# Kernel optimization log

Measured on AMD Instinct MI355X. Metric: run time of the kernel, lower is better.

The kernel has to match this reference:

```python
import jax, jax.numpy as jnp
import numpy as np

B, D, K, P = 512, 2048, 128, 5

def setup_inputs() -> dict:
    key = jax.random.key(0)
    k1, k2 = jax.random.split(key)
    x = jax.random.normal(k1, (B, D), dtype=jnp.float32)
    theta = 0.05 * jax.random.normal(k2, (D, K, P), dtype=jnp.float32)
    log_weight_scale = jnp.zeros((K, P), dtype=jnp.float32)
    bias = -jnp.ones((K,), dtype=jnp.float32)  # layer inits bias to -1
    return {"x": x, "theta": theta, "log_weight_scale": log_weight_scale, "bias": bias}

def reference(x, theta, log_weight_scale, bias):
    b = x.shape[0]
    # weight-normalized kernel: [D, K, P]
    norm = jnp.sqrt(jnp.sum(theta * theta, axis=0))            # [K, P]
    kernel = theta * (jnp.exp(log_weight_scale) / norm)[None]  # [D, K, P]
    actv = jnp.einsum('bd,dkp->bkp', x, kernel)                # [B, K, P]
    # pairwise L1 over P: [B, K, B]
    diff = jnp.abs(actv[:, :, :, None] - jnp.transpose(actv, (1, 2, 0))[None])  # [B,K,P,B]
    abs_dif = jnp.sum(diff, axis=2) + 1e6 * jnp.eye(b, dtype=x.dtype)[:, None, :]
    f = jnp.sum(jnp.exp(-abs_dif), axis=2) + bias[None, :]     # [B, K]
    return jnp.concatenate([x, f], axis=1)                     # [B, D+K]
```

## Files before the change

kernel.cpp:

```cpp
#include <hip/hip_runtime.h>
#include <math.h>

#define BSZ 512
#define DD 2048
#define KK 128
#define PP 5
#define NCOL (KK * PP)
#define OUTW (DD + KK)
#define LOG2E 1.4426950408889634f

#define KSPLIT 16
#define GK (DD / KSPLIT)
#define QSPLIT 8

typedef __attribute__((ext_vector_type(8))) short bf16x8;
typedef __attribute__((ext_vector_type(4))) float f32x4;

#define WS_NORM 0
#define WS_ACTV (WS_NORM + NCOL)
#define WS_FPART (WS_ACTV + BSZ * NCOL)
#define WS_XB (WS_FPART + QSPLIT * KK * BSZ)
#define WS_THT (WS_XB + BSZ * DD / 2)
#define WS_PART (WS_THT + NCOL * DD / 2)

__device__ inline ushort f2b(float f) {
    unsigned u = __float_as_uint(f);
    u += 0x7FFF + ((u >> 16) & 1);
    return (ushort)(u >> 16);
}

#define SWZ(r, c) ((((r) * 128) + ((c) ^ (((r) & 7) << 3))))

__global__ __launch_bounds__(256) void prep_kernel(const float* __restrict__ theta,
                                                   const float* __restrict__ x,
                                                   float* __restrict__ norm,
                                                   ushort* __restrict__ thT,
                                                   ushort* __restrict__ xb) {
    __shared__ float partial[32][8];
    __shared__ ushort sT[64][68];

    const int bid = blockIdx.x;
    const int t   = threadIdx.x;

    if (bid < 80) {
        const int c8  = bid * 8;
        const int col = c8 + (t & 7);
        const int g   = t >> 3;
        const float* p = theta + (size_t)g * NCOL + col;
        float s = 0.f;
#pragma unroll
        for (int j = 0; j < 64; ++j) {
            float v = p[(size_t)j * 32 * NCOL];
            s += v * v;
        }
        partial[g][t & 7] = s;
        __syncthreads();
        if (t < 8) {
            float acc = 0.f;
#pragma unroll
            for (int gg = 0; gg < 32; ++gg) acc += partial[gg][t];
            norm[c8 + t] = acc;
        }
    } else if (bid < 400) {
        const int tb    = bid - 80;
        const int kz    = (tb & 31) * 64;
        const int nz    = (tb >> 5) * 64;
        const int c4    = t & 15;
        const int rbase = t >> 4;
#pragma unroll
        for (int i = 0; i < 4; ++i) {
            int r = rbase + i * 16;
            float4 v = *(const float4*)&theta[(size_t)(kz + r) * NCOL + nz + c4 * 4];
            sT[c4 * 4 + 0][r] = f2b(v.x);
            sT[c4 * 4 + 1][r] = f2b(v.y);
            sT[c4 * 4 + 2][r] = f2b(v.z);
            sT[c4 * 4 + 3][r] = f2b(v.w);
        }
        __syncthreads();
#pragma unroll
        for (int i = 0; i < 2; ++i) {
            int slot = t + i * 256;
            int rr   = slot >> 3;
            int cc   = (slot & 7) * 8;
            ushort4 w0 = *(const ushort4*)&sT[rr][cc];
            ushort4 w1 = *(const ushort4*)&sT[rr][cc + 4];
            ushort* dst = &thT[(size_t)(nz + rr) * DD + kz + cc];
            *(ushort4*)&dst[0] = w0;
            *(ushort4*)&dst[4] = w1;
        }
    } else {
        const int b2 = bid - 400;
#pragma unroll
        for (int i = 0; i < 4; ++i) {
            int base = b2 * 4096 + i * 1024 + t * 4;
            float4 v = *(const float4*)&x[base];
            ushort4 w;
            w.x = f2b(v.x); w.y = f2b(v.y); w.z = f2b(v.z); w.w = f2b(v.w);
            *(ushort4*)&xb[base] = w;
        }
    }
}

__global__ __launch_bounds__(256) void gemm_kernel(const ushort* __restrict__ xb,
                                                   const ushort* __restrict__ thT,
                                                   ushort* __restrict__ parth,
                                                   const float* __restrict__ x,
                                                   float* __restrict__ out) {
    __shared__ ushort lA[64 * 128];
    __shared__ ushort lB[64 * 128];

    const int bx = blockIdx.x;
    if (bx >= 1280) {
        const int bid = bx - 1280;
        for (int i = bid * 256 + threadIdx.x; i < BSZ * (DD / 4); i += 80 * 256) {
            int r = i >> 9;
            int c = i & 511;
            float4 v = *(const float4*)&x[(size_t)r * DD + c * 4];
            *(float4*)&out[(size_t)r * OUTW + c * 4] = v;
        }
        return;
    }

    const int t    = threadIdx.x;
    const int lane = t & 63;
    const int wave = t >> 6;
    const int mt8  = bx & 7;
    const int rest = bx >> 3;
    const int bn   = (rest % 10) * 64;
    const int bm   = mt8 * 64;
    const int z    = rest / 10;
    const int kz   = z * GK;

    const ushort* gA = xb  + (size_t)bm * DD + kz;
    const ushort* gB = thT + (size_t)bn * DD + kz;

    const int srr = t >> 4;
    const int sss = t & 15;

    uint4 va[4], vb[4];
#pragma unroll
    for (int i = 0; i < 4; ++i) {
        int rr = srr + i * 16;
        va[i] = *(const uint4*)&gA[(size_t)rr * DD + sss * 8];
        vb[i] = *(const uint4*)&gB[(size_t)rr * DD + sss * 8];
    }
#pragma unroll
    for (int i = 0; i < 4; ++i) {
        int rr = srr + i * 16;
        *(uint4*)&lA[SWZ(rr, sss * 8)] = va[i];
        *(uint4*)&lB[SWZ(rr, sss * 8)] = vb[i];
    }
    __syncthreads();

    const int fr = lane & 15;
    const int g  = lane >> 4;
    const int mr = (wave >> 1) * 32 + fr;
    const int nr = (wave & 1) * 32 + fr;

    f32x4 acc[2][2] = {};
#pragma unroll
    for (int ks = 0; ks < 4; ++ks) {
        const int kc = ks * 32 + g * 8;
        bf16x8 a0 = *(const bf16x8*)&lA[SWZ(mr,      kc)];
        bf16x8 a1 = *(const bf16x8*)&lA[SWZ(mr + 16, kc)];
        bf16x8 b0 = *(const bf16x8*)&lB[SWZ(nr,      kc)];
        bf16x8 b1 = *(const bf16x8*)&lB[SWZ(nr + 16, kc)];
        acc[0][0] = __builtin_amdgcn_mfma_f32_16x16x32_bf16(a0, b0, acc[0][0], 0, 0, 0);
        acc[0][1] = __builtin_amdgcn_mfma_f32_16x16x32_bf16(a0, b1, acc[0][1], 0, 0, 0);
        acc[1][0] = __builtin_amdgcn_mfma_f32_16x16x32_bf16(a1, b0, acc[1][0], 0, 0, 0);
        acc[1][1] = __builtin_amdgcn_mfma_f32_16x16x32_bf16(a1, b1, acc[1][1], 0, 0, 0);
    }

    ushort* base = parth + (size_t)z * (BSZ * NCOL);
#pragma unroll
    for (int mt = 0; mt < 2; ++mt)
#pragma unroll
        for (int nt = 0; nt < 2; ++nt) {
            int row = bm + (wave >> 1) * 32 + mt * 16 + g * 4;
            int col = bn + (wave & 1) * 32 + nt * 16 + fr;
            ushort* dst = base + (size_t)row * NCOL + col;
#pragma unroll
            for (int reg = 0; reg < 4; ++reg)
                dst[(size_t)reg * NCOL] = f2b(acc[mt][nt][reg]);
        }
}

__global__ __launch_bounds__(256) void reduce_kernel(const ushort* __restrict__ parth,
                                                     const float* __restrict__ norm,
                                                     const float* __restrict__ lws,
                                                     float* __restrict__ actv) {
    int i = (blockIdx.x * 256 + threadIdx.x) * 2;
    float s0 = 0.f, s1 = 0.f;
#pragma unroll
    for (int q = 0; q < KSPLIT; ++q) {
        unsigned u = *(const unsigned*)&parth[(size_t)q * (BSZ * NCOL) + i];
        s0 += __uint_as_float(u << 16);
        s1 += __uint_as_float(u & 0xffff0000u);
    }
    const int col = i % NCOL;
    const float sc0 = __builtin_amdgcn_exp2f(lws[col] * LOG2E) *
                      __builtin_amdgcn_rsqf(norm[col]) * LOG2E;
    const float sc1 = __builtin_amdgcn_exp2f(lws[col + 1] * LOG2E) *
                      __builtin_amdgcn_rsqf(norm[col + 1]) * LOG2E;
    float2 o = make_float2(s0 * sc0, s1 * sc1);
    *(float2*)&actv[i] = o;
}

__global__ __launch_bounds__(256) void pairwise_kernel(const float* __restrict__ actv,
                                                       float* __restrict__ f_part) {
    const int k   = blockIdx.x;
    const int q   = blockIdx.y;
    const int tid = threadIdx.x;

    float a[2][PP];
#pragma unroll
    for (int r = 0; r < 2; ++r) {
        const float* ap = &actv[(size_t)(tid + r * 256) * NCOL + k * PP];
#pragma unroll
        for (int p = 0; p < PP; ++p) a[r][p] = ap[p];
    }

    const int ubase = __builtin_amdgcn_readfirstlane(q * 64 * NCOL + k * PP);
    const float* __restrict__ up = actv + ubase;

    float acc[2] = {0.f, 0.f};
#pragma unroll 8
    for (int j = 0; j < 64; ++j) {
        const float v0 = up[j * NCOL + 0];
        const float v1 = up[j * NCOL + 1];
        const float v2 = up[j * NCOL + 2];
        const float v3 = up[j * NCOL + 3];
        const float v4 = up[j * NCOL + 4];
#pragma unroll
        for (int r = 0; r < 2; ++r) {
            float s = fabsf(a[r][0] - v0) + fabsf(a[r][1] - v1) +
                      fabsf(a[r][2] - v2) + fabsf(a[r][3] - v3) +
                      fabsf(a[r][4] - v4);
            acc[r] += __builtin_amdgcn_exp2f(-s);
        }
    }

    float* fp = f_part + ((size_t)q * KK + k) * BSZ;
    fp[tid]       = acc[0];
    fp[tid + 256] = acc[1];
}

__global__ __launch_bounds__(256) void freduce_kernel(const float* __restrict__ f_part,
                                                      const float* __restrict__ bias,
                                                      float* __restrict__ out) {
    int i = blockIdx.x * 256 + threadIdx.x;
    int k = i >> 9;
    int b = i & 511;
    float s = 0.f;
#pragma unroll
    for (int q = 0; q < QSPLIT; ++q)
        s += f_part[((size_t)q * KK + k) * BSZ + b];
    out[(size_t)b * OUTW + DD + k] = s - 1.0f + bias[k];
}

extern "C" void kernel_launch(void* const* d_in, const int* in_sizes, int n_in,
                              void* d_out, int out_size, void* d_ws, size_t ws_size,
                              hipStream_t stream) {
    const float* x     = (const float*)d_in[0];
    const float* theta = (const float*)d_in[1];
    const float* lws   = (const float*)d_in[2];
    const float* bias  = (const float*)d_in[3];
    float* out = (float*)d_out;

    float* ws     = (float*)d_ws;
    float* norm   = ws + WS_NORM;
    float* actv   = ws + WS_ACTV;
    float* f_part = ws + WS_FPART;
    ushort* xb    = (ushort*)(ws + WS_XB);
    ushort* thT   = (ushort*)(ws + WS_THT);
    ushort* parth = (ushort*)(ws + WS_PART);

    prep_kernel<<<656, 256, 0, stream>>>(theta, x, norm, thT, xb);
    gemm_kernel<<<1360, 256, 0, stream>>>(xb, thT, parth, x, out);
    reduce_kernel<<<640, 256, 0, stream>>>(parth, norm, lws, actv);
    pairwise_kernel<<<dim3(KK, QSPLIT), 256, 0, stream>>>(actv, f_part);
    freduce_kernel<<<256, 256, 0, stream>>>(f_part, bias, out);
}
```

Before: 101.5 us.

## Fuse pairwise reduction into one kernel with LDS staging and k-major actv layout

The reduce kernel now writes actv in a k-major [K][B][P] layout, so each pairwise block loads its contiguous 512x5 column into shared memory. Each block handles 64 query rows, with four waves each covering 128 candidates, and reduces the partials in LDS before writing the final output with bias. This removes the separate freduce kernel launch and the f_part workspace round trip, and replaces strided global loads with LDS reads. The cost is scattered 4-byte stores in reduce_kernel and a block barrier for the LDS reduction.

```diff
diff --git a/kernel.cpp b/kernel.cpp
--- a/kernel.cpp
+++ b/kernel.cpp
@@ -11,15 +11,13 @@
 
 #define KSPLIT 16
 #define GK (DD / KSPLIT)
-#define QSPLIT 8
 
 typedef __attribute__((ext_vector_type(8))) short bf16x8;
 typedef __attribute__((ext_vector_type(4))) float f32x4;
 
 #define WS_NORM 0
 #define WS_ACTV (WS_NORM + NCOL)
-#define WS_FPART (WS_ACTV + BSZ * NCOL)
-#define WS_XB (WS_FPART + QSPLIT * KK * BSZ)
+#define WS_XB (WS_ACTV + BSZ * NCOL)
 #define WS_THT (WS_XB + BSZ * DD / 2)
 #define WS_PART (WS_THT + NCOL * DD / 2)
 
@@ -189,7 +187,9 @@
                                                      const float* __restrict__ norm,
                                                      const float* __restrict__ lws,
                                                      float* __restrict__ actv) {
-    int i = (blockIdx.x * 256 + threadIdx.x) * 2;
+    int i   = (blockIdx.x * 256 + threadIdx.x) * 2;
+    int b   = i / NCOL;
+    int col = i - b * NCOL;
     float s0 = 0.f, s1 = 0.f;
 #pragma unroll
     for (int q = 0; q < KSPLIT; ++q) {
@@ -197,65 +197,64 @@
         s0 += __uint_as_float(u << 16);
         s1 += __uint_as_float(u & 0xffff0000u);
     }
-    const int col = i % NCOL;
     const float sc0 = __builtin_amdgcn_exp2f(lws[col] * LOG2E) *
                       __builtin_amdgcn_rsqf(norm[col]) * LOG2E;
     const float sc1 = __builtin_amdgcn_exp2f(lws[col + 1] * LOG2E) *
                       __builtin_amdgcn_rsqf(norm[col + 1]) * LOG2E;
-    float2 o = make_float2(s0 * sc0, s1 * sc1);
-    *(float2*)&actv[i] = o;
+    int k0 = col / 5,       p0 = col - k0 * 5;
+    int k1 = (col + 1) / 5, p1 = (col + 1) - k1 * 5;
+    actv[((size_t)k0 * BSZ + b) * PP + p0] = s0 * sc0;
+    actv[((size_t)k1 * BSZ + b) * PP + p1] = s1 * sc1;
 }
 
 __global__ __launch_bounds__(256) void pairwise_kernel(const float* __restrict__ actv,
-                                                       float* __restrict__ f_part) {
+                                                       const float* __restrict__ bias,
+                                                       float* __restrict__ out) {
     const int k   = blockIdx.x;
-    const int q   = blockIdx.y;
+    const int bc  = blockIdx.y;
     const int tid = threadIdx.x;
-
-    float a[2][PP];
-#pragma unroll
-    for (int r = 0; r < 2; ++r) {
-        const float* ap = &actv[(size_t)(tid + r * 256) * NCOL + k * PP];
-#pragma unroll
-        for (int p = 0; p < PP; ++p) a[r][p] = ap[p];
-    }
-
-    const int ubase = __builtin_amdgcn_readfirstlane(q * 64 * NCOL + k * PP);
-    const float* __restrict__ up = actv + ubase;
-
-    float acc[2] = {0.f, 0.f};
+    const int r   = tid & 63;
+    const int seg = tid >> 6;
+
+    __shared__ float sB[512][8];
+    __shared__ float red[4][64];
+
+    const float* col = actv + (size_t)k * (BSZ * PP);
+
+    for (int i = tid; i < BSZ * PP; i += 256) {
+        int rr = i / 5;
+        sB[rr][i - rr * 5] = col[i];
+    }
+
+    const int b = bc * 64 + r;
+    const float a0 = col[b * 5 + 0];
+    const float a1 = col[b * 5 + 1];
+    const float a2 = col[b * 5 + 2];
+    const float a3 = col[b * 5 + 3];
+    const float a4 = col[b * 5 + 4];
+    __syncthreads();
+
+    float acc0 = 0.f, acc1 = 0.f;
+    const int j0 = seg * 128;
 #pragma unroll 8
-    for (int j = 0; j < 64; ++j) {
-        const float v0 = up[j * NCOL + 0];
-        const float v1 = up[j * NCOL + 1];
-        const float v2 = up[j * NCOL + 2];
-        const float v3 = up[j * NCOL + 3];
-        const float v4 = up[j * NCOL + 4];
-#pragma unroll
-        for (int r = 0; r < 2; ++r) {
-            float s = fabsf(a[r][0] - v0) + fabsf(a[r][1] - v1) +
-                      fabsf(a[r][2] - v2) + fabsf(a[r][3] - v3) +
-                      fabsf(a[r][4] - v4);
-            acc[r] += __builtin_amdgcn_exp2f(-s);
-        }
-    }
-
-    float* fp = f_part + ((size_t)q * KK + k) * BSZ;
-    fp[tid]       = acc[0];
-    fp[tid + 256] = acc[1];
-}
-
-__global__ __launch_bounds__(256) void freduce_kernel(const float* __restrict__ f_part,
-                                                      const float* __restrict__ bias,
-                                                      float* __restrict__ out) {
-    int i = blockIdx.x * 256 + threadIdx.x;
-    int k = i >> 9;
-    int b = i & 511;
-    float s = 0.f;
-#pragma unroll
-    for (int q = 0; q < QSPLIT; ++q)
-        s += f_part[((size_t)q * KK + k) * BSZ + b];
-    out[(size_t)b * OUTW + DD + k] = s - 1.0f + bias[k];
+    for (int jj = 0; jj < 128; jj += 2) {
+        const float4 v  = *(const float4*)&sB[j0 + jj][0];
+        const float  v4 = sB[j0 + jj][4];
+        float s = fabsf(a0 - v.x) + fabsf(a1 - v.y) + fabsf(a2 - v.z) +
+                  fabsf(a3 - v.w) + fabsf(a4 - v4);
+        acc0 += __builtin_amdgcn_exp2f(-s);
+        const float4 w  = *(const float4*)&sB[j0 + jj + 1][0];
+        const float  w4 = sB[j0 + jj + 1][4];
+        float t = fabsf(a0 - w.x) + fabsf(a1 - w.y) + fabsf(a2 - w.z) +
+                  fabsf(a3 - w.w) + fabsf(a4 - w4);
+        acc1 += __builtin_amdgcn_exp2f(-t);
+    }
+    red[seg][r] = acc0 + acc1;
+    __syncthreads();
+    if (tid < 64) {
+        float s = red[0][tid] + red[1][tid] + red[2][tid] + red[3][tid];
+        out[(size_t)(bc * 64 + tid) * OUTW + DD + k] = s - 1.0f + bias[k];
+    }
 }
 
 extern "C" void kernel_launch(void* const* d_in, const int* in_sizes, int n_in,
@@ -270,7 +269,6 @@
     float* ws     = (float*)d_ws;
     float* norm   = ws + WS_NORM;
     float* actv   = ws + WS_ACTV;
-    float* f_part = ws + WS_FPART;
     ushort* xb    = (ushort*)(ws + WS_XB);
     ushort* thT   = (ushort*)(ws + WS_THT);
     ushort* parth = (ushort*)(ws + WS_PART);
@@ -278,6 +276,5 @@
     prep_kernel<<<656, 256, 0, stream>>>(theta, x, norm, thT, xb);
     gemm_kernel<<<1360, 256, 0, stream>>>(xb, thT, parth, x, out);
     reduce_kernel<<<640, 256, 0, stream>>>(parth, norm, lws, actv);
-    pairwise_kernel<<<dim3(KK, QSPLIT), 256, 0, stream>>>(actv, f_part);
-    freduce_kernel<<<256, 256, 0, stream>>>(f_part, bias, out);
-}
+    pairwise_kernel<<<dim3(KK, 8), 256, 0, stream>>>(actv, bias, out);
+}
```

New measurement: 102.1 us. About the same (+0.6%).
